# Optimization experiments

Hardware: AMD Instinct MI355X
Metric: run time of the kernel (lower is better)

## Reference

```python
import jax, jax.numpy as jnp
import numpy as np
from jax import lax

N, D, H = 4096, 768, 16384


def setup_inputs() -> dict:
    key = jax.random.key(0)
    k0, k1, k2, k3, k4, k5, k6 = jax.random.split(key, 7)
    bound_e = 1.0 / np.sqrt(D)   # kaiming_uniform(a=sqrt(5)) on (H, D) -> bound 1/sqrt(fan_in)
    bound_d = 1.0 / np.sqrt(H)   # nn.Linear default init, fan_in = H
    return {
        "vision_embeddings": jax.random.normal(k0, (N, D), dtype=jnp.float32),
        "text_embeddings": jax.random.normal(k1, (N, D), dtype=jnp.float32),
        "encoder": jax.random.uniform(k2, (H, D), jnp.float32, -bound_e, bound_e),
        "Wv": jax.random.uniform(k3, (D, H), jnp.float32, -bound_d, bound_d),
        "bv": jax.random.uniform(k4, (D,), jnp.float32, -bound_d, bound_d),
        "Wt": jax.random.uniform(k5, (D, H), jnp.float32, -bound_d, bound_d),
        "bt": jax.random.uniform(k6, (D,), jnp.float32, -bound_d, bound_d),
        "topk": 32,
    }


def _l2norm(x, axis):
    return x / jnp.maximum(jnp.linalg.norm(x, axis=axis, keepdims=True), 1e-12)


def _encode(emb, encoder, topk):
    # F.normalize rows, then cdist(p=2) between unit vectors: ||a-b|| = sqrt(2-2 a.b)
    w = _l2norm(encoder, axis=1)            # [H, D]
    e = _l2norm(emb, axis=1)                # [N, D]
    cos = jnp.einsum("nd,hd->nh", e, w)     # [N, H]
    dist = jnp.sqrt(jnp.maximum(2.0 - 2.0 * cos, 0.0))
    sim = 2.0 - dist                         # [N, H]
    # kthvalue(abs, k=H-topk) == (topk+1)-th largest; keep strictly-greater entries
    abs_f = jnp.abs(sim)
    thres = lax.top_k(abs_f, topk + 1)[0][:, -1]  # [N]
    mask = (abs_f > thres[:, None]).astype(sim.dtype)
    return sim * mask


def reference(vision_embeddings, text_embeddings, encoder, Wv, bv, Wt, bt, topk):
    latent_v = _encode(vision_embeddings, encoder, topk)          # [N, H]
    recon_v = jnp.einsum("nh,dh->nd", latent_v, Wv) + bv          # [N, D]
    latent_t = _encode(text_embeddings, encoder, topk)            # [N, H]
    recon_t = jnp.einsum("nh,dh->nd", latent_t, Wt) + bt          # [N, D]
    return (recon_v, recon_t, latent_v, latent_t)
```

## Files before the change

### kernel.cpp

```cpp
#include <hip/hip_runtime.h>
#include <math.h>


#define N_ROWS 4096
#define D_DIM  768
#define H_DIM  16384
#define M_TOT  8192
#define TOPK   32
#define MARGIN 1e-3f
#define SEL_CAP 40
#define AMB_CAP 64
#define CAP2   512

typedef __attribute__((ext_vector_type(8))) short short8;
typedef __attribute__((ext_vector_type(4))) float floatx4;

__device__ inline unsigned short bf16_rne(float f) {
    unsigned u = __float_as_uint(f);
    unsigned r = u + 0x7fffu + ((u >> 16) & 1u);
    return (unsigned short)(r >> 16);
}

__device__ inline void gload16(const unsigned short* g, unsigned short* l) {
    __builtin_amdgcn_global_load_lds(
        (const __attribute__((address_space(1))) void*)g,
        (__attribute__((address_space(3))) void*)l, 16, 0, 0);
}

__global__ void split_all_kernel(const float* __restrict__ embv,
                                 const float* __restrict__ embt,
                                 const float* __restrict__ enc,
                                 unsigned short* __restrict__ Ahi,
                                 unsigned short* __restrict__ Alo,
                                 unsigned short* __restrict__ Bh,
                                 float* __restrict__ invA,
                                 float* __restrict__ invB)
{
    int row = blockIdx.x;
    int tid = threadIdx.x;
    const float* src;
    unsigned short *hi, *lo;
    float* invp;
    if (row < N_ROWS) {
        src = embv + (size_t)row * D_DIM;
        hi = Ahi + (size_t)row * D_DIM; lo = Alo + (size_t)row * D_DIM;
        invp = invA + row;
    } else if (row < 2 * N_ROWS) {
        int r = row - N_ROWS;
        src = embt + (size_t)r * D_DIM;
        hi = Ahi + (size_t)row * D_DIM; lo = Alo + (size_t)row * D_DIM;
        invp = invA + row;
    } else {
        int r = row - 2 * N_ROWS;
        src = enc + (size_t)r * D_DIM;
        hi = Bh + (size_t)r * D_DIM; lo = nullptr;
        invp = invB + r;
    }
    __shared__ float red[4];
    const float4* s4 = reinterpret_cast<const float4*>(src);
    float4 v = make_float4(0.f, 0.f, 0.f, 0.f);
    float ss = 0.f;
    if (tid < 192) {
        v = s4[tid];
        ss = v.x * v.x + v.y * v.y + v.z * v.z + v.w * v.w;
    }
    #pragma unroll
    for (int o = 32; o > 0; o >>= 1) ss += __shfl_down(ss, o);
    int wave = tid >> 6, lane = tid & 63;
    if (lane == 0) red[wave] = ss;
    __syncthreads();
    if (tid == 0) {
        float tot = red[0] + red[1] + red[2];
        red[0] = 1.f / fmaxf(sqrtf(tot), 1e-12f);
    }
    __syncthreads();
    float inv = red[0];
    if (tid == 0) *invp = inv;
    if (tid < 192) {
        float x[4] = {v.x * inv, v.y * inv, v.z * inv, v.w * inv};
        unsigned short hh[4], ll[4];
        #pragma unroll
        for (int t = 0; t < 4; t++) {
            hh[t] = bf16_rne(x[t]);
            float hf = __uint_as_float((unsigned)hh[t] << 16);
            ll[t] = bf16_rne(x[t] - hf);
        }
        ushort4 h4; h4.x = hh[0]; h4.y = hh[1]; h4.z = hh[2]; h4.w = hh[3];
        *reinterpret_cast<ushort4*>(hi + tid * 4) = h4;
        if (lo) {
            ushort4 l4; l4.x = ll[0]; l4.y = ll[1]; l4.z = ll[2]; l4.w = ll[3];
            *reinterpret_cast<ushort4*>(lo + tid * 4) = l4;
        }
    }
}

#define GBK 32
#define NTILE (D_DIM / GBK)

__global__ __launch_bounds__(256, 3)
void gemm_mfma_kernel(const unsigned short* __restrict__ Ahi,
                      const unsigned short* __restrict__ Alo,
                      const unsigned short* __restrict__ Bh,
                      float* __restrict__ latent)
{
    __shared__ unsigned short sA[2][2][128 * GBK];
    __shared__ unsigned short sB[2][128 * GBK];

    int tid = threadIdx.x;
    int lane = tid & 63;
    int wave = tid >> 6;
    int wr = (wave >> 1) * 64;
    int wc = (wave & 1) * 64;
    int m = lane & 15;
    int q = lane >> 4;

    unsigned nwgx = gridDim.x;
    unsigned lid = blockIdx.y * nwgx + blockIdx.x;
    unsigned cpx = (nwgx * gridDim.y) >> 3;
    unsigned swz = (lid & 7u) * cpx + (lid >> 3);
    int bx = (int)(swz % nwgx);
    int by = (int)(swz / nwgx);

    int row0 = by * 128;
    int col0 = bx * 128;

    int p0 = tid, p1 = tid + 256;
    int r0 = ((p0 >> 5) << 3) | (p0 & 7), q0 = (p0 >> 3) & 3;
    int r1 = ((p1 >> 5) << 3) | (p1 & 7), q1 = (p1 >> 3) & 3;
    size_t aoff0 = (size_t)(row0 + r0) * D_DIM + q0 * 8;
    size_t aoff1 = (size_t)(row0 + r1) * D_DIM + q1 * 8;
    size_t boff0 = (size_t)(col0 + r0) * D_DIM + q0 * 8;
    size_t boff1 = (size_t)(col0 + r1) * D_DIM + q1 * 8;

    int am0 = wr + m;
    int bn0 = wc + m;
    int offA = ((am0 >> 3) << 8) + (q << 6) + ((am0 & 7) << 3);
    int offB = ((bn0 >> 3) << 8) + (q << 6) + ((bn0 & 7) << 3);

    floatx4 acc[4][4];
    #pragma unroll
    for (int i = 0; i < 4; i++)
        #pragma unroll
        for (int j = 0; j < 4; j++)
            acc[i][j] = (floatx4){0.f, 0.f, 0.f, 0.f};

    auto stage = [&](int t, int b) {
        int k0 = t * GBK;
        gload16(Ahi + aoff0 + k0, &sA[b][0][p0 * 8]);
        gload16(Ahi + aoff1 + k0, &sA[b][0][p1 * 8]);
        gload16(Alo + aoff0 + k0, &sA[b][1][p0 * 8]);
        gload16(Alo + aoff1 + k0, &sA[b][1][p1 * 8]);
        gload16(Bh + boff0 + k0, &sB[b][p0 * 8]);
        gload16(Bh + boff1 + k0, &sB[b][p1 * 8]);
    };

    auto compute = [&](int b) {
        short8 fah[4], fal[4], fbv[4];
        #pragma unroll
        for (int i = 0; i < 4; i++) {
            fah[i] = *(const short8*)&sA[b][0][offA + i * 512];
            fal[i] = *(const short8*)&sA[b][1][offA + i * 512];
        }
        #pragma unroll
        for (int j = 0; j < 4; j++)
            fbv[j] = *(const short8*)&sB[b][offB + j * 512];
        __builtin_amdgcn_s_setprio(1);
        #pragma unroll
        for (int j = 0; j < 4; j++) {
            #pragma unroll
            for (int i = 0; i < 4; i++) {
                acc[i][j] = __builtin_amdgcn_mfma_f32_16x16x32_bf16(fah[i], fbv[j], acc[i][j], 0, 0, 0);
                acc[i][j] = __builtin_amdgcn_mfma_f32_16x16x32_bf16(fal[i], fbv[j], acc[i][j], 0, 0, 0);
            }
        }
        __builtin_amdgcn_s_setprio(0);
    };

    stage(0, 0);
    int cur = 0;
    for (int t = 0; t < NTILE - 1; ++t) {
        stage(t + 1, cur ^ 1);
        asm volatile("s_waitcnt vmcnt(6)" ::: "memory");
        __builtin_amdgcn_s_barrier();
        __builtin_amdgcn_sched_barrier(0);
        compute(cur);
        __builtin_amdgcn_sched_barrier(0);
        __builtin_amdgcn_s_barrier();
        cur ^= 1;
    }
    asm volatile("s_waitcnt vmcnt(0)" ::: "memory");
    __builtin_amdgcn_s_barrier();
    __builtin_amdgcn_sched_barrier(0);
    compute(cur);

    #pragma unroll
    for (int i = 0; i < 4; i++) {
        #pragma unroll
        for (int r = 0; r < 4; r++) {
            int grow = row0 + wr + i * 16 + q * 4 + r;
            float* dst = latent + (size_t)grow * H_DIM + col0 + wc + m;
            #pragma unroll
            for (int j = 0; j < 4; j++) {
                float cosv = acc[i][j][r];
                float sim = 2.f - sqrtf(fmaxf(2.f - 2.f * cosv, 0.f));
                __builtin_nontemporal_store(sim, dst + j * 16);
            }
        }
    }
}

__global__ __launch_bounds__(256)
void select_kernel(float* __restrict__ latent,
                   int* __restrict__ sel_cnt,
                   int* __restrict__ sel_idx,
                   float* __restrict__ sel_val,
                   int* __restrict__ amb_cnt,
                   int* __restrict__ amb_idx)
{
    int row = blockIdx.x;
    int tid = threadIdx.x;
    float* v = latent + (size_t)row * H_DIM;
    const floatx4* v4 = (const floatx4*)v;
    floatx4* vw = (floatx4*)v;

    __shared__ _Float16 hbuf[H_DIM];
    __shared__ float smax[256];
    __shared__ float sca[CAP2];
    __shared__ int   sci[CAP2];
    __shared__ float sT;
    __shared__ int scnt, svstar, skept, samb;

    float mx = -1.f;
    #pragma unroll 4
    for (int k = 0; k < 16; k++) {
        int i = tid + 256 * k;
        floatx4 x = __builtin_nontemporal_load(&v4[i]);
        float a0 = fabsf(x.x), a1 = fabsf(x.y), a2 = fabsf(x.z), a3 = fabsf(x.w);
        hbuf[4 * i + 0] = (_Float16)a0;
        hbuf[4 * i + 1] = (_Float16)a1;
        hbuf[4 * i + 2] = (_Float16)a2;
        hbuf[4 * i + 3] = (_Float16)a3;
        mx = fmaxf(mx, fmaxf(fmaxf(a0, a1), fmaxf(a2, a3)));
    }
    smax[tid] = mx;
    if (tid == 0) { scnt = 0; svstar = 0x7FFFFFFF; skept = 0; samb = 0; }
    __syncthreads();

    int gt = 0;
    for (int j = 0; j < 256; j++) {
        float mj = smax[j];
        gt += (mj > mx || (mj == mx && j < tid)) ? 1 : 0;
    }
    if (gt == 32) sT = mx;
    __syncthreads();
    float Tm = sT - MARGIN;

    #pragma unroll 4
    for (int k = 0; k < 16; k++) {
        int i = tid + 256 * k;
        float a[4];
        a[0] = (float)hbuf[4 * i + 0]; a[1] = (float)hbuf[4 * i + 1];
        a[2] = (float)hbuf[4 * i + 2]; a[3] = (float)hbuf[4 * i + 3];
        bool any = (a[0] >= Tm) | (a[1] >= Tm) | (a[2] >= Tm) | (a[3] >= Tm);
        if (any) {
            #pragma unroll
            for (int t = 0; t < 4; t++) {
                if (a[t] >= Tm) {
                    int c = atomicAdd(&scnt, 1);
                    if (c < CAP2) { sci[c] = 4 * i + t; sca[c] = v[4 * i + t]; }
                }
            }
        }
        floatx4 zz = (floatx4){0.f, 0.f, 0.f, 0.f};
        __builtin_nontemporal_store(zz, &vw[i]);
    }
    __syncthreads();

    int C = min(scnt, CAP2);
    for (int c = tid; c < C; c += 256) {
        float a = fabsf(sca[c]);
        int g = 0;
        for (int j = 0; j < C; j++) {
            float aj = fabsf(sca[j]);
            g += (aj > a || (aj == a && j < c)) ? 1 : 0;
        }
        if (g <= TOPK) atomicMin(&svstar, __float_as_int(a));
    }
    __syncthreads();
    float vs = __int_as_float(svstar);

    for (int c = tid; c < C; c += 256) {
        float f = sca[c];
        float a = fabsf(f);
        int idx = sci[c];
        if (a > vs + MARGIN) {
            int s = atomicAdd(&skept, 1);
            sel_idx[(size_t)row * SEL_CAP + s] = idx;
            sel_val[(size_t)row * SEL_CAP + s] = f;
            v[idx] = f;
        } else if (a >= vs - MARGIN) {
            int s = atomicAdd(&samb, 1);
            if (s < AMB_CAP) amb_idx[(size_t)row * AMB_CAP + s] = idx;
        }
    }
    __syncthreads();
    if (tid == 0) { sel_cnt[row] = skept; amb_cnt[row] = min(samb, AMB_CAP); }
}

__global__ void refine_kernel(const float* __restrict__ embv,
                              const float* __restrict__ embt,
                              const float* __restrict__ enc,
                              const float* __restrict__ invA,
                              const float* __restrict__ invB,
                              float* __restrict__ latent,
                              int* __restrict__ sel_cnt,
                              int* __restrict__ sel_idx,
                              float* __restrict__ sel_val,
                              const int* __restrict__ amb_cnt,
                              const int* __restrict__ amb_idx)
{
    int row = blockIdx.x;
    int s = amb_cnt[row];
    if (s == 0) return;
    int tid = threadIdx.x;
    int m = sel_cnt[row];
    int need = TOPK - m;
    float* v = latent + (size_t)row * H_DIM;
    if (need <= 0) return;
    __shared__ float ex[AMB_CAP];
    __shared__ int evs, kc;
    const float* src = (row < N_ROWS) ? embv + (size_t)row * D_DIM
                                      : embt + (size_t)(row - N_ROWS) * D_DIM;
    float ia = invA[row];
    int wave = tid >> 6, lane = tid & 63;
    for (int a = wave; a < s; a += 4) {
        int h = amb_idx[(size_t)row * AMB_CAP + a];
        const float* w = enc + (size_t)h * D_DIM;
        float d = 0.f;
        for (int t = lane; t < D_DIM; t += 64) d += src[t] * w[t];
        #pragma unroll
        for (int o = 32; o > 0; o >>= 1) d += __shfl_down(d, o);
        if (lane == 0) {
            float cosv = d * ia * invB[h];
            ex[a] = 2.f - sqrtf(fmaxf(2.f - 2.f * cosv, 0.f));
        }
    }
    if (tid == 0) { evs = 0x7FFFFFFF; kc = 0; }
    __syncthreads();
    if (tid < s) {
        float mya = fabsf(ex[tid]);
        int g = 0;
        for (int j = 0; j < s; j++) {
            float aj = fabsf(ex[j]);
            g += (aj > mya || (aj == mya && j < tid)) ? 1 : 0;
        }
        if (g <= need) atomicMin(&evs, __float_as_int(mya));
    }
    __syncthreads();
    float ep = __int_as_float(evs);
    if (tid < s) {
        int idx = amb_idx[(size_t)row * AMB_CAP + tid];
        float e = ex[tid];
        if (fabsf(e) > ep) {
            int sl = atomicAdd(&kc, 1);
            v[idx] = e;
            sel_idx[(size_t)row * SEL_CAP + m + sl] = idx;
            sel_val[(size_t)row * SEL_CAP + m + sl] = e;
        }
    }
    __syncthreads();
    if (tid == 0) sel_cnt[row] = m + kc;
}

__global__ void transpose_kernel(const float* __restrict__ Wv,
                                 const float* __restrict__ Wt,
                                 float* __restrict__ WvT,
                                 float* __restrict__ WtT)
{
    int z = blockIdx.z;
    const float* W = z ? Wt : Wv;
    float* WT = z ? WtT : WvT;
    __shared__ float tile[32][33];
    int tx = threadIdx.x & 31;
    int ty = threadIdx.x >> 5;
    int h0 = blockIdx.x * 32;
    int d0 = blockIdx.y * 32;
    #pragma unroll
    for (int t = 0; t < 4; t++)
        tile[ty + t * 8][tx] = W[(size_t)(d0 + ty + t * 8) * H_DIM + h0 + tx];
    __syncthreads();
    #pragma unroll
    for (int t = 0; t < 4; t++)
        WT[(size_t)(h0 + ty + t * 8) * D_DIM + d0 + tx] = tile[tx][ty + t * 8];
}

__global__ void recon_kernel(const float* __restrict__ Wv_,
                             const float* __restrict__ Wt_,
                             const float* __restrict__ bv,
                             const float* __restrict__ bt,
                             const int* __restrict__ sel_cnt,
                             const int* __restrict__ sel_idx,
                             const float* __restrict__ sel_val,
                             long sh, long sd,
                             float* __restrict__ out)
{
    int n = blockIdx.x;
    int z = blockIdx.y;
    int row = z * N_ROWS + n;
    const float* W = z ? Wt_ : Wv_;
    const float* bias = z ? bt : bv;
    float* o = out + (size_t)z * N_ROWS * D_DIM + (size_t)n * D_DIM;

    __shared__ int s_idx[SEL_CAP];
    __shared__ float s_val[SEL_CAP];
    __shared__ int s_cnt;
    int tid = threadIdx.x;
    if (tid == 0) s_cnt = sel_cnt[row];
    __syncthreads();
    int cnt = s_cnt;
    if (tid < cnt) {
        s_idx[tid] = sel_idx[(size_t)row * SEL_CAP + tid];
        s_val[tid] = sel_val[(size_t)row * SEL_CAP + tid];
    }
    __syncthreads();

    for (int d = tid; d < D_DIM; d += 256) {
        float acc = bias[d];
        for (int j = 0; j < cnt; j++)
            acc += s_val[j] * W[(size_t)s_idx[j] * sh + (size_t)d * sd];
        o[d] = acc;
    }
}

__global__ void row_invnorm_kernel(const float* __restrict__ x,
                                   float* __restrict__ inv, int rows) {
    int row = blockIdx.x * 4 + (threadIdx.x >> 6);
    int lane = threadIdx.x & 63;
    if (row >= rows) return;
    const float4* p = reinterpret_cast<const float4*>(x + (size_t)row * D_DIM);
    float ss = 0.f;
    #pragma unroll
    for (int i = 0; i < 3; i++) {
        float4 v = p[lane + i * 64];
        ss += v.x * v.x + v.y * v.y + v.z * v.z + v.w * v.w;
    }
    #pragma unroll
    for (int off = 32; off > 0; off >>= 1) ss += __shfl_down(ss, off);
    if (lane == 0) inv[row] = 1.f / fmaxf(sqrtf(ss), 1e-12f);
}

#define BM 128
#define BN 128
#define BK 16
__global__ __launch_bounds__(256)
void gemm_sim_kernel(const float* __restrict__ embv,
                     const float* __restrict__ embt,
                     const float* __restrict__ enc,
                     const float* __restrict__ inv_emb,
                     const float* __restrict__ inv_enc,
                     float* __restrict__ latent)
{
    int z = blockIdx.z;
    const float* A = z ? embt : embv;
    const float* invA = inv_emb + z * N_ROWS;
    float* C = latent + (size_t)z * N_ROWS * H_DIM;
    __shared__ float As[BK][BM + 4];
    __shared__ float Bs[BK][BN + 4];
    int tid = threadIdx.x;
    int tx = tid & 15, ty = tid >> 4;
    int row0 = blockIdx.y * BM, col0 = blockIdx.x * BN;
    float acc[8][8];
    #pragma unroll
    for (int i = 0; i < 8; i++)
        #pragma unroll
        for (int j = 0; j < 8; j++) acc[i][j] = 0.f;
    for (int k0 = 0; k0 < D_DIM; k0 += BK) {
        #pragma unroll
        for (int t = 0; t < 2; t++) {
            int idx = t * 256 + tid;
            int r = idx >> 2, c4 = idx & 3;
            float4 va = *reinterpret_cast<const float4*>(
                A + (size_t)(row0 + r) * D_DIM + k0 + c4 * 4);
            As[c4 * 4 + 0][r] = va.x; As[c4 * 4 + 1][r] = va.y;
            As[c4 * 4 + 2][r] = va.z; As[c4 * 4 + 3][r] = va.w;
            float4 vb = *reinterpret_cast<const float4*>(
                enc + (size_t)(col0 + r) * D_DIM + k0 + c4 * 4);
            Bs[c4 * 4 + 0][r] = vb.x; Bs[c4 * 4 + 1][r] = vb.y;
            Bs[c4 * 4 + 2][r] = vb.z; Bs[c4 * 4 + 3][r] = vb.w;
        }
        __syncthreads();
        #pragma unroll
        for (int kk = 0; kk < BK; kk++) {
            float a[8], b[8];
            *reinterpret_cast<float4*>(&a[0]) = *reinterpret_cast<const float4*>(&As[kk][ty * 8]);
            *reinterpret_cast<float4*>(&a[4]) = *reinterpret_cast<const float4*>(&As[kk][ty * 8 + 4]);
            *reinterpret_cast<float4*>(&b[0]) = *reinterpret_cast<const float4*>(&Bs[kk][tx * 8]);
            *reinterpret_cast<float4*>(&b[4]) = *reinterpret_cast<const float4*>(&Bs[kk][tx * 8 + 4]);
            #pragma unroll
            for (int i = 0; i < 8; i++)
                #pragma unroll
                for (int j = 0; j < 8; j++)
                    acc[i][j] = fmaf(a[i], b[j], acc[i][j]);
        }
        __syncthreads();
    }
    #pragma unroll
    for (int i = 0; i < 8; i++) {
        int n = row0 + ty * 8 + i;
        float sa = invA[n];
        float* Crow = C + (size_t)n * H_DIM + col0 + tx * 8;
        float tmp[8];
        #pragma unroll
        for (int j = 0; j < 8; j++) {
            float cosv = acc[i][j] * sa * inv_enc[col0 + tx * 8 + j];
            tmp[j] = 2.f - sqrtf(fmaxf(2.f - 2.f * cosv, 0.f));
        }
        float4 o0 = {tmp[0], tmp[1], tmp[2], tmp[3]};
        float4 o1 = {tmp[4], tmp[5], tmp[6], tmp[7]};
        *reinterpret_cast<float4*>(Crow) = o0;
        *reinterpret_cast<float4*>(Crow + 4) = o1;
    }
}

__global__ void legacy_select_kernel(float* __restrict__ latent,
                                     const int* __restrict__ topk_p,
                                     int* __restrict__ sel_cnt,
                                     int* __restrict__ sel_idx,
                                     float* __restrict__ sel_val)
{
    int row = blockIdx.x;
    float* v = latent + (size_t)row * H_DIM;
    int tid = threadIdx.x;
    __shared__ unsigned hist[256];
    __shared__ unsigned s_prefix;
    __shared__ int s_k;
    __shared__ int s_cnt;
    int k = topk_p[0] + 1;
    unsigned prefix = 0;
    for (int shift = 24; shift >= 0; shift -= 8) {
        hist[tid] = 0;
        __syncthreads();
        unsigned pmask = (shift == 24) ? 0u : (0xFFFFFFFFu << (shift + 8));
        for (int i = tid; i < H_DIM; i += 256) {
            unsigned u = __float_as_uint(v[i]) & 0x7FFFFFFFu;
            if ((u & pmask) == prefix)
                atomicAdd(&hist[(u >> shift) & 255u], 1u);
        }
        __syncthreads();
        if (tid == 0) {
            int c = 0, b = 255;
            for (; b >= 0; b--) {
                c += (int)hist[b];
                if (c >= k) break;
            }
            if (b < 0) b = 0;
            s_prefix = prefix | ((unsigned)b << shift);
            s_k = k - (c - (int)hist[b]);
        }
        __syncthreads();
        prefix = s_prefix;
        k = s_k;
        __syncthreads();
    }
    float thres = __uint_as_float(prefix);
    if (tid == 0) s_cnt = 0;
    __syncthreads();
    for (int i = tid; i < H_DIM; i += 256) {
        float x = v[i];
        bool keep = (fabsf(x) > thres);
        v[i] = keep ? x : 0.f;
        if (keep) {
            int slot = atomicAdd(&s_cnt, 1);
            if (slot < SEL_CAP) {
                sel_idx[(size_t)row * SEL_CAP + slot] = i;
                sel_val[(size_t)row * SEL_CAP + slot] = x;
            }
        }
    }
    __syncthreads();
    if (tid == 0) sel_cnt[row] = (s_cnt > SEL_CAP) ? SEL_CAP : s_cnt;
}

extern "C" void kernel_launch(void* const* d_in, const int* in_sizes, int n_in,
                              void* d_out, int out_size, void* d_ws, size_t ws_size,
                              hipStream_t stream) {
    const float* embv = (const float*)d_in[0];
    const float* embt = (const float*)d_in[1];
    const float* enc  = (const float*)d_in[2];
    const float* Wv   = (const float*)d_in[3];
    const float* bv   = (const float*)d_in[4];
    const float* Wt   = (const float*)d_in[5];
    const float* bt   = (const float*)d_in[6];
    const int* topk   = (const int*)d_in[7];
    float* out = (float*)d_out;

    float* recon_out = out;
    float* latent = out + (size_t)2 * N_ROWS * D_DIM;

    char* ws = (char*)d_ws;
    size_t off = 0;
    float* invA = (float*)(ws + off);            off += (size_t)M_TOT * 4;
    float* invB = (float*)(ws + off);            off += (size_t)H_DIM * 4;
    int*   sel_cnt = (int*)(ws + off);           off += (size_t)M_TOT * 4;
    int*   amb_cnt = (int*)(ws + off);           off += (size_t)M_TOT * 4;
    int*   sel_idx = (int*)(ws + off);           off += (size_t)M_TOT * SEL_CAP * 4;
    float* sel_val = (float*)(ws + off);         off += (size_t)M_TOT * SEL_CAP * 4;
    int*   amb_idx = (int*)(ws + off);           off += (size_t)M_TOT * AMB_CAP * 4;
    unsigned short* Ahi = (unsigned short*)(ws + off); off += (size_t)M_TOT * D_DIM * 2;
    unsigned short* Alo = (unsigned short*)(ws + off); off += (size_t)M_TOT * D_DIM * 2;
    unsigned short* Bh  = (unsigned short*)(ws + off); off += (size_t)H_DIM * D_DIM * 2;
    size_t core_need = off;
    float* WvT = (float*)(ws + off);
    float* WtT = WvT + (size_t)D_DIM * H_DIM;
    size_t full_need = off + (size_t)2 * D_DIM * H_DIM * 4;

    if (ws_size >= core_need) {
        bool use_T = ws_size >= full_need;

        split_all_kernel<<<2 * N_ROWS + H_DIM, 256, 0, stream>>>(
            embv, embt, enc, Ahi, Alo, Bh, invA, invB);

        gemm_mfma_kernel<<<dim3(H_DIM / 128, M_TOT / 128), 256, 0, stream>>>(
            Ahi, Alo, Bh, latent);

        select_kernel<<<M_TOT, 256, 0, stream>>>(latent,
            sel_cnt, sel_idx, sel_val, amb_cnt, amb_idx);

        refine_kernel<<<M_TOT, 256, 0, stream>>>(embv, embt, enc, invA, invB,
            latent, sel_cnt, sel_idx, sel_val, amb_cnt, amb_idx);

        if (use_T) {
            transpose_kernel<<<dim3(H_DIM / 32, D_DIM / 32, 2), 256, 0, stream>>>(
                Wv, Wt, WvT, WtT);
            recon_kernel<<<dim3(N_ROWS, 2), 256, 0, stream>>>(
                WvT, WtT, bv, bt, sel_cnt, sel_idx, sel_val, (long)D_DIM, 1L, recon_out);
        } else {
            recon_kernel<<<dim3(N_ROWS, 2), 256, 0, stream>>>(
                Wv, Wt, bv, bt, sel_cnt, sel_idx, sel_val, 1L, (long)H_DIM, recon_out);
        }
    } else {
        size_t o2 = 0;
        float* inv_enc = (float*)(ws + o2); o2 += (size_t)H_DIM * 4;
        float* inv_emb = (float*)(ws + o2); o2 += (size_t)2 * N_ROWS * 4;
        int*   l_cnt = (int*)(ws + o2);     o2 += (size_t)2 * N_ROWS * 4;
        int*   l_idx = (int*)(ws + o2);     o2 += (size_t)2 * N_ROWS * SEL_CAP * 4;
        float* l_val = (float*)(ws + o2);   o2 += (size_t)2 * N_ROWS * SEL_CAP * 4;
        row_invnorm_kernel<<<H_DIM / 4, 256, 0, stream>>>(enc, inv_enc, H_DIM);
        row_invnorm_kernel<<<N_ROWS / 4, 256, 0, stream>>>(embv, inv_emb, N_ROWS);
        row_invnorm_kernel<<<N_ROWS / 4, 256, 0, stream>>>(embt, inv_emb + N_ROWS, N_ROWS);
        dim3 g(H_DIM / BN, N_ROWS / BM, 2);
        gemm_sim_kernel<<<g, 256, 0, stream>>>(embv, embt, enc, inv_emb, inv_enc, latent);
        legacy_select_kernel<<<2 * N_ROWS, 256, 0, stream>>>(latent, topk, l_cnt, l_idx, l_val);
        recon_kernel<<<dim3(N_ROWS, 2), 256, 0, stream>>>(
            Wv, Wt, bv, bt, l_cnt, l_idx, l_val, 1L, (long)H_DIM, recon_out);
    }
}
```

Before: 1.583 ms.

## Emit thresholded top-k candidates from GEMM epilogue instead of full latent

```diff
diff --git a/kernel.cpp b/kernel.cpp
--- a/kernel.cpp
+++ b/kernel.cpp
@@ -10,7 +10,9 @@
 #define MARGIN 1e-3f
 #define SEL_CAP 40
 #define AMB_CAP 64
-#define CAP2   512
+#define CCAP   512
+#define THR_COS 0.08f
+#define THR_SIM_GUARD 0.6436f
 
 typedef __attribute__((ext_vector_type(8))) short short8;
 typedef __attribute__((ext_vector_type(4))) float floatx4;
@@ -25,6 +27,19 @@
     __builtin_amdgcn_global_load_lds(
         (const __attribute__((address_space(1))) void*)g,
         (__attribute__((address_space(3))) void*)l, 16, 0, 0);
+}
+
+__global__ __launch_bounds__(256)
+void zero_fill_kernel(floatx4* __restrict__ lat4, long n4,
+                      int* __restrict__ cnts, int ncnt)
+{
+    long i = (long)blockIdx.x * 256 + threadIdx.x;
+    long stride = (long)gridDim.x * 256;
+    floatx4 z = (floatx4){0.f, 0.f, 0.f, 0.f};
+    for (long p = i; p < n4; p += stride)
+        __builtin_nontemporal_store(z, &lat4[p]);
+    for (long p = i; p < ncnt; p += stride)
+        cnts[p] = 0;
 }
 
 __global__ void split_all_kernel(const float* __restrict__ embv,
@@ -101,7 +116,9 @@
 void gemm_mfma_kernel(const unsigned short* __restrict__ Ahi,
                       const unsigned short* __restrict__ Alo,
                       const unsigned short* __restrict__ Bh,
-                      float* __restrict__ latent)
+                      int* __restrict__ cand_cnt,
+                      int* __restrict__ cand_idx,
+                      float* __restrict__ cand_val)
 {
     __shared__ unsigned short sA[2][2][128 * GBK];
     __shared__ unsigned short sB[2][128 * GBK];
@@ -198,90 +215,58 @@
         #pragma unroll
         for (int r = 0; r < 4; r++) {
             int grow = row0 + wr + i * 16 + q * 4 + r;
-            float* dst = latent + (size_t)grow * H_DIM + col0 + wc + m;
             #pragma unroll
             for (int j = 0; j < 4; j++) {
                 float cosv = acc[i][j][r];
-                float sim = 2.f - sqrtf(fmaxf(2.f - 2.f * cosv, 0.f));
-                __builtin_nontemporal_store(sim, dst + j * 16);
+                if (cosv >= THR_COS) {
+                    int slot = atomicAdd(&cand_cnt[grow], 1);
+                    if (slot < CCAP) {
+                        cand_idx[(size_t)grow * CCAP + slot] = col0 + wc + m + j * 16;
+                        cand_val[(size_t)grow * CCAP + slot] = cosv;
+                    }
+                }
             }
         }
     }
 }
 
 __global__ __launch_bounds__(256)
-void select_kernel(float* __restrict__ latent,
-                   int* __restrict__ sel_cnt,
-                   int* __restrict__ sel_idx,
-                   float* __restrict__ sel_val,
-                   int* __restrict__ amb_cnt,
-                   int* __restrict__ amb_idx)
+void cand_select_kernel(const int* __restrict__ cand_cnt,
+                        const int* __restrict__ cand_idx,
+                        const float* __restrict__ cand_val,
+                        float* __restrict__ latent,
+                        int* __restrict__ sel_cnt,
+                        int* __restrict__ sel_idx,
+                        float* __restrict__ sel_val,
+                        int* __restrict__ amb_cnt,
+                        int* __restrict__ amb_idx,
+                        int* __restrict__ flag)
 {
     int row = blockIdx.x;
     int tid = threadIdx.x;
-    float* v = latent + (size_t)row * H_DIM;
-    const floatx4* v4 = (const floatx4*)v;
-    floatx4* vw = (floatx4*)v;
-
-    __shared__ _Float16 hbuf[H_DIM];
-    __shared__ float smax[256];
-    __shared__ float sca[CAP2];
-    __shared__ int   sci[CAP2];
-    __shared__ float sT;
-    __shared__ int scnt, svstar, skept, samb;
-
-    float mx = -1.f;
-    #pragma unroll 4
-    for (int k = 0; k < 16; k++) {
-        int i = tid + 256 * k;
-        floatx4 x = __builtin_nontemporal_load(&v4[i]);
-        float a0 = fabsf(x.x), a1 = fabsf(x.y), a2 = fabsf(x.z), a3 = fabsf(x.w);
-        hbuf[4 * i + 0] = (_Float16)a0;
-        hbuf[4 * i + 1] = (_Float16)a1;
-        hbuf[4 * i + 2] = (_Float16)a2;
-        hbuf[4 * i + 3] = (_Float16)a3;
-        mx = fmaxf(mx, fmaxf(fmaxf(a0, a1), fmaxf(a2, a3)));
-    }
-    smax[tid] = mx;
-    if (tid == 0) { scnt = 0; svstar = 0x7FFFFFFF; skept = 0; samb = 0; }
-    __syncthreads();
-
-    int gt = 0;
-    for (int j = 0; j < 256; j++) {
-        float mj = smax[j];
-        gt += (mj > mx || (mj == mx && j < tid)) ? 1 : 0;
-    }
-    if (gt == 32) sT = mx;
-    __syncthreads();
-    float Tm = sT - MARGIN;
-
-    #pragma unroll 4
-    for (int k = 0; k < 16; k++) {
-        int i = tid + 256 * k;
-        float a[4];
-        a[0] = (float)hbuf[4 * i + 0]; a[1] = (float)hbuf[4 * i + 1];
-        a[2] = (float)hbuf[4 * i + 2]; a[3] = (float)hbuf[4 * i + 3];
-        bool any = (a[0] >= Tm) | (a[1] >= Tm) | (a[2] >= Tm) | (a[3] >= Tm);
-        if (any) {
-            #pragma unroll
-            for (int t = 0; t < 4; t++) {
-                if (a[t] >= Tm) {
-                    int c = atomicAdd(&scnt, 1);
-                    if (c < CAP2) { sci[c] = 4 * i + t; sca[c] = v[4 * i + t]; }
-                }
-            }
-        }
-        floatx4 zz = (floatx4){0.f, 0.f, 0.f, 0.f};
-        __builtin_nontemporal_store(zz, &vw[i]);
-    }
-    __syncthreads();
-
-    int C = min(scnt, CAP2);
-    for (int c = tid; c < C; c += 256) {
-        float a = fabsf(sca[c]);
+    int cnt = cand_cnt[row];
+
+    __shared__ float sv[CCAP];
+    __shared__ int   si[CCAP];
+    __shared__ int svstar, skept, samb;
+
+    if (cnt > CCAP || cnt < TOPK + 1) {
+        if (tid == 0) { flag[row] = 1; sel_cnt[row] = 0; amb_cnt[row] = 0; }
+        return;
+    }
+    for (int c = tid; c < cnt; c += 256) {
+        float cosv = cand_val[(size_t)row * CCAP + c];
+        sv[c] = 2.f - sqrtf(fmaxf(2.f - 2.f * cosv, 0.f));
+        si[c] = cand_idx[(size_t)row * CCAP + c];
+    }
+    if (tid == 0) { svstar = 0x7FFFFFFF; skept = 0; samb = 0; }
+    __syncthreads();
+
+    for (int c = tid; c < cnt; c += 256) {
+        float a = sv[c];
         int g = 0;
-        for (int j = 0; j < C; j++) {
-            float aj = fabsf(sca[j]);
+        for (int j = 0; j < cnt; j++) {
+            float aj = sv[j];
             g += (aj > a || (aj == a && j < c)) ? 1 : 0;
         }
         if (g <= TOPK) atomicMin(&svstar, __float_as_int(a));
@@ -289,22 +274,111 @@
     __syncthreads();
     float vs = __int_as_float(svstar);
 
-    for (int c = tid; c < C; c += 256) {
-        float f = sca[c];
-        float a = fabsf(f);
-        int idx = sci[c];
-        if (a > vs + MARGIN) {
+    if (vs - MARGIN <= THR_SIM_GUARD) {
+        if (tid == 0) { flag[row] = 1; sel_cnt[row] = 0; amb_cnt[row] = 0; }
+        return;
+    }
+
+    for (int c = tid; c < cnt; c += 256) {
+        float f = sv[c];
+        int idx = si[c];
+        if (f > vs + MARGIN) {
             int s = atomicAdd(&skept, 1);
             sel_idx[(size_t)row * SEL_CAP + s] = idx;
             sel_val[(size_t)row * SEL_CAP + s] = f;
-            v[idx] = f;
-        } else if (a >= vs - MARGIN) {
+            latent[(size_t)row * H_DIM + idx] = f;
+        } else if (f >= vs - MARGIN) {
             int s = atomicAdd(&samb, 1);
             if (s < AMB_CAP) amb_idx[(size_t)row * AMB_CAP + s] = idx;
         }
     }
     __syncthreads();
     if (tid == 0) { sel_cnt[row] = skept; amb_cnt[row] = min(samb, AMB_CAP); }
+}
+
+__global__ __launch_bounds__(256)
+void fallback_kernel(const int* __restrict__ flag,
+                     const float* __restrict__ embv,
+                     const float* __restrict__ embt,
+                     const float* __restrict__ enc,
+                     const float* __restrict__ invA,
+                     const float* __restrict__ invB,
+                     float* __restrict__ latent,
+                     int* __restrict__ sel_cnt,
+                     int* __restrict__ sel_idx,
+                     float* __restrict__ sel_val,
+                     int* __restrict__ amb_cnt)
+{
+    int row = blockIdx.x;
+    if (!flag[row]) return;
+    int tid = threadIdx.x;
+    float* v = latent + (size_t)row * H_DIM;
+    __shared__ float ssrc[D_DIM];
+    __shared__ unsigned hist[256];
+    __shared__ unsigned s_prefix;
+    __shared__ int s_k, s_cnt;
+
+    const float* src = (row < N_ROWS) ? embv + (size_t)row * D_DIM
+                                      : embt + (size_t)(row - N_ROWS) * D_DIM;
+    for (int d = tid; d < D_DIM; d += 256) ssrc[d] = src[d];
+    float ia = invA[row];
+    __syncthreads();
+    for (int h = tid; h < H_DIM; h += 256) {
+        const float* w = enc + (size_t)h * D_DIM;
+        float d = 0.f;
+        for (int t = 0; t < D_DIM; t++) d += ssrc[t] * w[t];
+        float cosv = d * ia * invB[h];
+        v[h] = 2.f - sqrtf(fmaxf(2.f - 2.f * cosv, 0.f));
+    }
+    __syncthreads();
+
+    int k = TOPK + 1;
+    unsigned prefix = 0;
+    for (int shift = 24; shift >= 0; shift -= 8) {
+        hist[tid] = 0;
+        __syncthreads();
+        unsigned pmask = (shift == 24) ? 0u : (0xFFFFFFFFu << (shift + 8));
+        for (int i = tid; i < H_DIM; i += 256) {
+            unsigned u = __float_as_uint(v[i]);
+            if ((u & pmask) == prefix)
+                atomicAdd(&hist[(u >> shift) & 255u], 1u);
+        }
+        __syncthreads();
+        if (tid == 0) {
+            int c = 0, b = 255;
+            for (; b >= 0; b--) {
+                c += (int)hist[b];
+                if (c >= k) break;
+            }
+            if (b < 0) b = 0;
+            s_prefix = prefix | ((unsigned)b << shift);
+            s_k = k - (c - (int)hist[b]);
+        }
+        __syncthreads();
+        prefix = s_prefix;
+        k = s_k;
+        __syncthreads();
+    }
+    float thres = __uint_as_float(prefix);
+    if (tid == 0) s_cnt = 0;
+    __syncthreads();
+    for (int i = tid; i < H_DIM; i += 256) {
+        float x = v[i];
+        bool keep = (x > thres);
+        v[i] = keep ? x : 0.f;
+        if (keep) {
+            int slot = atomicAdd(&s_cnt, 1);
+            if (slot < SEL_CAP) {
+                sel_idx[(size_t)row * SEL_CAP + slot] = i;
+                sel_val[(size_t)row * SEL_CAP + slot] = x;
+            }
+        }
+    }
+    __syncthreads();
+    if (tid == 0) {
+        sel_cnt[row] = (s_cnt > SEL_CAP) ? SEL_CAP : s_cnt;
+        amb_cnt[row] = 0;
+    }
 }
 
 __global__ void refine_kernel(const float* __restrict__ embv,
@@ -606,25 +680,40 @@
     int*   sel_idx = (int*)(ws + off);           off += (size_t)M_TOT * SEL_CAP * 4;
     float* sel_val = (float*)(ws + off);         off += (size_t)M_TOT * SEL_CAP * 4;
     int*   amb_idx = (int*)(ws + off);           off += (size_t)M_TOT * AMB_CAP * 4;
+    int*   cand_cnt = (int*)(ws + off);          off += (size_t)M_TOT * 4;
+    int*   flag     = (int*)(ws + off);          off += (size_t)M_TOT * 4;
     unsigned short* Ahi = (unsigned short*)(ws + off); off += (size_t)M_TOT * D_DIM * 2;
     unsigned short* Alo = (unsigned short*)(ws + off); off += (size_t)M_TOT * D_DIM * 2;
     unsigned short* Bh  = (unsigned short*)(ws + off); off += (size_t)H_DIM * D_DIM * 2;
     size_t core_need = off;
+
+    int*   cand_idx = (int*)(ws + off);
+    float* cand_val = (float*)(ws + off + (size_t)M_TOT * CCAP * 4);
+    size_t cand_bytes = (size_t)M_TOT * CCAP * 8;
     float* WvT = (float*)(ws + off);
     float* WtT = WvT + (size_t)D_DIM * H_DIM;
-    size_t full_need = off + (size_t)2 * D_DIM * H_DIM * 4;
-
-    if (ws_size >= core_need) {
-        bool use_T = ws_size >= full_need;
+    size_t trans_bytes = (size_t)2 * D_DIM * H_DIM * 4;
+
+    if (ws_size >= core_need + cand_bytes) {
+        bool use_T = ws_size >= core_need + trans_bytes;
 
         split_all_kernel<<<2 * N_ROWS + H_DIM, 256, 0, stream>>>(
             embv, embt, enc, Ahi, Alo, Bh, invA, invB);
 
+        zero_fill_kernel<<<2048, 256, 0, stream>>>(
+            (floatx4*)latent, (long)((size_t)2 * N_ROWS * H_DIM / 4),
+            cand_cnt, 2 * M_TOT);
+
         gemm_mfma_kernel<<<dim3(H_DIM / 128, M_TOT / 128), 256, 0, stream>>>(
-            Ahi, Alo, Bh, latent);
-
-        select_kernel<<<M_TOT, 256, 0, stream>>>(latent,
-            sel_cnt, sel_idx, sel_val, amb_cnt, amb_idx);
+            Ahi, Alo, Bh, cand_cnt, cand_idx, cand_val);
+
+        cand_select_kernel<<<M_TOT, 256, 0, stream>>>(
+            cand_cnt, cand_idx, cand_val, latent,
+            sel_cnt, sel_idx, sel_val, amb_cnt, amb_idx, flag);
+
+        fallback_kernel<<<M_TOT, 256, 0, stream>>>(
+            flag, embv, embt, enc, invA, invB, latent,
+            sel_cnt, sel_idx, sel_val, amb_cnt);
 
         refine_kernel<<<M_TOT, 256, 0, stream>>>(embv, embt, enc, invA, invB,
             latent, sel_cnt, sel_idx, sel_val, amb_cnt, amb_idx);
```

Measured after the change: 2.022 ms. 27.7% more time.
